# Optimization experiments

Hardware: AMD Instinct MI355X
Metric: run time of the kernel (lower is better)

Reference implementation:

```python
import jax, jax.numpy as jnp
import numpy as np

N = 50000      # nodes
E = 800000     # edges
IN = 128       # input features (arxiv)
HID = 128      # hidden per head
HEADS = 3      # arxiv_data=True -> 3 heads
OUT = 40       # classes
EPS = 1e-5     # BN eps
SLOPE = 0.2    # DGL GATConv leaky_relu negative slope


def setup_inputs() -> dict:
    key = jax.random.key(0)
    ks = jax.random.split(key, 20)
    x = jax.random.normal(ks[0], (N, IN), jnp.float32)
    src = jax.random.randint(ks[1], (E,), 0, N, dtype=jnp.int32)
    # guarantee every node has >=1 in-edge so edge_softmax is well-defined
    dst = jnp.concatenate([jnp.arange(N, dtype=jnp.int32),
                           jax.random.randint(ks[2], (E - N,), 0, N, dtype=jnp.int32)])

    def lin(k, fi, fo):
        return jax.random.normal(k, (fi, fo), jnp.float32) * (1.0 / np.sqrt(fi))

    def attn(k, h, d):
        return jax.random.normal(k, (h, d), jnp.float32) * 0.1

    return {
        "x": x, "src": src, "dst": dst,
        # layer 0: IN -> HEADS*HID
        "W0": lin(ks[3], IN, HEADS * HID),
        "al0": attn(ks[4], HEADS, HID), "ar0": attn(ks[5], HEADS, HID),
        "b0": jnp.zeros((HEADS * HID,), jnp.float32),
        # layer 1: HEADS*HID -> HEADS*HID
        "W1": lin(ks[6], HEADS * HID, HEADS * HID),
        "al1": attn(ks[7], HEADS, HID), "ar1": attn(ks[8], HEADS, HID),
        "b1": jnp.zeros((HEADS * HID,), jnp.float32),
        # layer 2: HEADS*HID -> OUT, 1 head
        "W2": lin(ks[9], HEADS * HID, OUT),
        "al2": attn(ks[10], 1, OUT), "ar2": attn(ks[11], 1, OUT),
        "b2": jnp.zeros((OUT,), jnp.float32),
        # batch norms over HEADS*HID channels
        "g0": jnp.ones((HEADS * HID,), jnp.float32), "be0": jnp.zeros((HEADS * HID,), jnp.float32),
        "g1": jnp.ones((HEADS * HID,), jnp.float32), "be1": jnp.zeros((HEADS * HID,), jnp.float32),
    }


def gat_layer(h, src, dst, W, al, ar, b, heads, d_out):
    # fc + per-head split: [N, heads, d_out]
    f = (h @ W).reshape(-1, heads, d_out)
    el = jnp.einsum('nhd,hd->nh', f, al)          # [N, H]
    er = jnp.einsum('nhd,hd->nh', f, ar)          # [N, H]
    e = jax.nn.leaky_relu(el[src] + er[dst], SLOPE)  # [E, H]
    # edge softmax over incoming edges of each dst node
    m = jax.ops.segment_max(e, dst, num_segments=N)
    ex = jnp.exp(e - m[dst])
    s = jax.ops.segment_sum(ex, dst, num_segments=N)
    a = ex / s[dst]                                # [E, H]
    # u_mul_e + sum aggregation
    out = jax.ops.segment_sum(f[src] * a[:, :, None], dst, num_segments=N)  # [N, H, D]
    out = out + b.reshape(1, heads, d_out)
    return out.reshape(-1, heads * d_out)


def batch_norm(h, g, b):
    mu = h.mean(axis=0)
    var = h.var(axis=0)
    return g * (h - mu) / jnp.sqrt(var + EPS) + b


def reference(x, src, dst, W0, al0, ar0, b0, W1, al1, ar1, b1,
              W2, al2, ar2, b2, g0, be0, g1, be1):
    h = gat_layer(x, src, dst, W0, al0, ar0, b0, HEADS, HID)
    h = jax.nn.relu(batch_norm(h, g0, be0))        # dropout: eval mode (identity)
    h = gat_layer(h, src, dst, W1, al1, ar1, b1, HEADS, HID)
    h = jax.nn.relu(batch_norm(h, g1, be1))
    out = gat_layer(h, src, dst, W2, al2, ar2, b2, 1, OUT)
    return out
```

## Files before the change

### kernel.cpp

```cpp
#include <hip/hip_runtime.h>
#include <hip/hip_bf16.h>

typedef __hip_bfloat16 bf16;
typedef __attribute__((ext_vector_type(8))) short short8;
typedef __attribute__((ext_vector_type(4))) float f32x4;

static constexpr int N_NODES  = 50000;
static constexpr int N_EDGES  = 800000;
static constexpr int F_IN     = 128;
static constexpr int D_HID    = 128;
static constexpr int H_HEADS  = 3;
static constexpr int F_OUT    = 40;
static constexpr int DEG_CAP  = 64;
static constexpr float BN_EPS = 1e-5f;
static constexpr float SLOPE  = 0.2f;

__device__ __forceinline__ float bfLo(unsigned int u) { return __uint_as_float(u << 16); }
__device__ __forceinline__ float bfHi(unsigned int u) { return __uint_as_float(u & 0xffff0000u); }
__device__ __forceinline__ float bfs(unsigned short s) { return __uint_as_float(((unsigned int)s) << 16); }
__device__ __forceinline__ unsigned int packbf(float a, float b) {
  union { bf16 h[2]; unsigned int u; } pk;
  pk.h[0] = __float2bfloat16(a);
  pk.h[1] = __float2bfloat16(b);
  return pk.u;
}
__device__ __forceinline__ short f2bf_s(float v) {
  bf16 h = __float2bfloat16(v);
  union { bf16 b; short s; } c; c.b = h; return c.s;
}
__device__ __forceinline__ void unpack_i8x4(unsigned int w, float* v) {
  v[0] = (float)(int)(char)(w & 0xff);
  v[1] = (float)(int)(char)((w >> 8) & 0xff);
  v[2] = (float)(int)(char)((w >> 16) & 0xff);
  v[3] = (float)(int)(char)((w >> 24) & 0xff);
}

__global__ __launch_bounds__(256) void gemm_mfma(const short* __restrict__ A,
                                                 const short* __restrict__ WT,
                                                 bf16* __restrict__ C,
                                                 const float* __restrict__ alp,
                                                 const float* __restrict__ arp,
                                                 float* __restrict__ el,
                                                 float* __restrict__ er,
                                                 const float* __restrict__ bnsrc,
                                                 const float* __restrict__ g,
                                                 const float* __restrict__ be,
                                                 float* __restrict__ bnstats,
                                                 int M, int K, int Nc, int els, int ers,
                                                 int lda, int ldc, int adiag) {
  constexpr int BM = 128, BN = 128, BK = 64, LDP = BK + 8;
  __shared__ short As[BM * LDP];
  __shared__ short Bs[BN * LDP];
  __shared__ float ecomb[128][4];
  __shared__ float sscale[384];
  __shared__ float sshift[384];
  int tid = threadIdx.x;
  int wave = tid >> 6, lane = tid & 63;
  int bm = blockIdx.y, bn = blockIdx.x;
  int m15 = lane & 15, quad = lane >> 4;
  int ksub = quad * 8;
  int wr = wave >> 1, wc = wave & 1;
  int srow = tid >> 3;
  int scol = (tid & 7) * 8;
  int acol0 = adiag ? bn * K : 0;

  if (bnsrc) {
    float inv_n = 1.f / (float)M;
    for (int c = tid; c < K; c += 256) {
      float mu = bnsrc[c] * inv_n;
      float var = bnsrc[K + c] * inv_n - mu * mu;
      float s = g[c] * rsqrtf(var + BN_EPS);
      sscale[c] = s;
      sshift[c] = be[c] - mu * s;
    }
    __syncthreads();
  }

  f32x4 acc[4][4];
#pragma unroll
  for (int i = 0; i < 4; ++i)
#pragma unroll
    for (int j = 0; j < 4; ++j) acc[i][j] = (f32x4){0.f, 0.f, 0.f, 0.f};

  for (int k0 = 0; k0 < K; k0 += BK) {
    int cb = k0 + scol;
    f32x4 sc0, sc1, sh0, sh1;
    if (bnsrc) {
      sc0 = *(const f32x4*)&sscale[cb]; sc1 = *(const f32x4*)&sscale[cb + 4];
      sh0 = *(const f32x4*)&sshift[cb]; sh1 = *(const f32x4*)&sshift[cb + 4];
    }
#pragma unroll
    for (int c = 0; c < 4; ++c) {
      int r = srow + c * 32;
      int gr = bm * BM + r; if (gr >= M) gr = M - 1;
      short8 av = *(const short8*)&A[(size_t)gr * lda + acol0 + k0 + scol];
      if (bnsrc) {
#pragma unroll
        for (int j = 0; j < 8; ++j) {
          float v = bfs((unsigned short)av[j]);
          float s = (j < 4) ? ((const float*)&sc0)[j] : ((const float*)&sc1)[j - 4];
          float t = (j < 4) ? ((const float*)&sh0)[j] : ((const float*)&sh1)[j - 4];
          float y = v * s + t;
          av[j] = f2bf_s(y > 0.f ? y : 0.f);
        }
      }
      *(short8*)&As[r * LDP + scol] = av;
      int gn = bn * BN + r;
      *(short8*)&Bs[r * LDP + scol] = *(const short8*)&WT[(size_t)gn * K + k0 + scol];
    }
    __syncthreads();
#pragma unroll
    for (int ks = 0; ks < BK; ks += 32) {
      short8 a[4], b[4];
#pragma unroll
      for (int i = 0; i < 4; ++i)
        a[i] = *(const short8*)&As[(wr * 64 + i * 16 + m15) * LDP + ks + ksub];
#pragma unroll
      for (int j = 0; j < 4; ++j)
        b[j] = *(const short8*)&Bs[(wc * 64 + j * 16 + m15) * LDP + ks + ksub];
#pragma unroll
      for (int i = 0; i < 4; ++i)
#pragma unroll
        for (int j = 0; j < 4; ++j)
          acc[i][j] = __builtin_amdgcn_mfma_f32_16x16x32_bf16(a[i], b[j], acc[i][j], 0, 0, 0);
    }
    __syncthreads();
  }

  int h = bn;
  float alv[4], arv[4];
#pragma unroll
  for (int j = 0; j < 4; ++j) {
    int col = bn * BN + wc * 64 + j * 16 + m15;
    alv[j] = alp[col];
    arv[j] = arp[col];
  }
  float csum[4] = {0.f, 0.f, 0.f, 0.f}, csq[4] = {0.f, 0.f, 0.f, 0.f};
#pragma unroll
  for (int i = 0; i < 4; ++i) {
#pragma unroll
    for (int r = 0; r < 4; ++r) {
      int rl = wr * 64 + i * 16 + quad * 4 + r;
      int row = bm * BM + rl;
      float pe = 0.f, pr = 0.f;
#pragma unroll
      for (int j = 0; j < 4; ++j) {
        float v = acc[i][j][r];
        pe += v * alv[j];
        pr += v * arv[j];
        if (bnstats && row < M) { csum[j] += v; csq[j] += v * v; }
        int col = bn * BN + wc * 64 + j * 16 + m15;
        if (row < M && col < Nc)
          C[(size_t)row * ldc + col] = __float2bfloat16(v);
      }
#pragma unroll
      for (int off = 1; off < 16; off <<= 1) {
        pe += __shfl_xor(pe, off);
        pr += __shfl_xor(pr, off);
      }
      if (m15 == 0) {
        ecomb[rl][wc] = pe;
        ecomb[rl][2 + wc] = pr;
      }
    }
  }
  if (bnstats) {
#pragma unroll
    for (int j = 0; j < 4; ++j) {
      csum[j] += __shfl_xor(csum[j], 16); csum[j] += __shfl_xor(csum[j], 32);
      csq[j]  += __shfl_xor(csq[j], 16);  csq[j]  += __shfl_xor(csq[j], 32);
    }
    if (quad == 0) {
#pragma unroll
      for (int j = 0; j < 4; ++j) {
        int col = bn * BN + wc * 64 + j * 16 + m15;
        atomicAdd(bnstats + col, csum[j]);
        atomicAdd(bnstats + Nc + col, csq[j]);
      }
    }
  }
  __syncthreads();
  if (tid < 128) {
    int row = bm * BM + tid;
    if (row < M) {
      el[(size_t)row * els + h] = ecomb[tid][0] + ecomb[tid][1];
      er[(size_t)row * ers + h] = ecomb[tid][2] + ecomb[tid][3];
    }
  }
}

__global__ void prep_kernel(const float* __restrict__ x, bf16* __restrict__ abuf,
                            const float* __restrict__ W0, const float* __restrict__ W1,
                            const float* __restrict__ W2, bf16* __restrict__ WT0,
                            bf16* __restrict__ WT1, bf16* __restrict__ WT2,
                            const float* __restrict__ al2, const float* __restrict__ ar2,
                            float* __restrict__ alp2, float* __restrict__ arp2,
                            int* __restrict__ fill, float* __restrict__ bnzero,
                            const float* __restrict__ al0, const float* __restrict__ ar0,
                            float* __restrict__ vl, float* __restrict__ vr) {
  const int NTOT = N_NODES * F_IN;
  for (int i = blockIdx.x * blockDim.x + threadIdx.x; i < NTOT;
       i += gridDim.x * blockDim.x) {
    abuf[i] = __float2bfloat16(x[i]);
    if (i < 384 * 384) { int n = i / 384, k = i - n * 384; WT1[i] = __float2bfloat16(W1[(size_t)k * 384 + n]); }
    if (i < 384 * 128) { int n = i / 128, k = i - n * 128; WT0[i] = __float2bfloat16(W0[(size_t)k * 384 + n]); }
    if (i < 128 * 384) { int n = i / 384, k = i - n * 384; WT2[i] = __float2bfloat16(n < F_OUT ? W2[(size_t)k * F_OUT + n] : 0.f); }
    if (i < N_NODES) fill[i] = 0;
    if (i < 4 * 384) bnzero[i] = 0.f;
    if (i < 128) { alp2[i] = i < F_OUT ? al2[i] : 0.f; arp2[i] = i < F_OUT ? ar2[i] : 0.f; }
  }
  if (blockIdx.x < 96) {
    int wid = blockIdx.x * 4 + (threadIdx.x >> 6);
    int lane = threadIdx.x & 63;
    int h = wid >> 7, k = wid & 127;
    const float2* wrow = (const float2*)(W0 + (size_t)k * 384 + h * 128);
    const float2* av = (const float2*)(al0 + h * 128);
    const float2* rv = (const float2*)(ar0 + h * 128);
    float2 wv = wrow[lane], a2 = av[lane], r2 = rv[lane];
    float sl = wv.x * a2.x + wv.y * a2.y;
    float sr = wv.x * r2.x + wv.y * r2.y;
#pragma unroll
    for (int off = 32; off > 0; off >>= 1) {
      sl += __shfl_xor(sl, off);
      sr += __shfl_xor(sr, off);
    }
    if (lane == 0) { vl[wid] = sl; vr[wid] = sr; }
  }
}

__global__ __launch_bounds__(256) void elr_kernel(const unsigned int* __restrict__ x2,
                                                  const float* __restrict__ vl,
                                                  const float* __restrict__ vr,
                                                  float* __restrict__ el,
                                                  float* __restrict__ er,
                                                  const int* __restrict__ src,
                                                  const int* __restrict__ dst,
                                                  int* __restrict__ fill,
                                                  int* __restrict__ bucket,
                                                  unsigned short* __restrict__ xq8,
                                                  float* __restrict__ xscale,
                                                  int N, int E) {
  int gid = blockIdx.x * 256 + threadIdx.x;
  if (gid < E) {
    int d = dst[gid];
    int pos = atomicAdd(fill + d, 1);
    if (pos < DEG_CAP) bucket[(size_t)d * DEG_CAP + pos] = src[gid];
  }
  int wv = threadIdx.x >> 6, lane = threadIdx.x & 63;
  int n = blockIdx.x * 4 + wv;
  if (n >= N) return;
  unsigned int u = x2[(size_t)n * 64 + lane];
  float v0 = bfLo(u), v1 = bfHi(u);
  float mx = fmaxf(fabsf(v0), fabsf(v1));
#pragma unroll
  for (int off = 32; off > 0; off >>= 1) mx = fmaxf(mx, __shfl_xor(mx, off));
  float qinv = mx > 0.f ? 127.f / mx : 0.f;
  int q0 = (int)rintf(v0 * qinv), q1 = (int)rintf(v1 * qinv);
  xq8[(size_t)n * 64 + lane] = (unsigned short)((q0 & 0xff) | ((q1 & 0xff) << 8));
  if (lane == 0) xscale[n] = mx * (1.f / 127.f);
  float pl[3], pr[3];
#pragma unroll
  for (int h = 0; h < 3; ++h) {
    float2 a2 = *(const float2*)&vl[h * 128 + 2 * lane];
    float2 r2 = *(const float2*)&vr[h * 128 + 2 * lane];
    pl[h] = v0 * a2.x + v1 * a2.y;
    pr[h] = v0 * r2.x + v1 * r2.y;
  }
#pragma unroll
  for (int h = 0; h < 3; ++h) {
#pragma unroll
    for (int off = 32; off > 0; off >>= 1) {
      pl[h] += __shfl_xor(pl[h], off);
      pr[h] += __shfl_xor(pr[h], off);
    }
  }
  if (lane == 0) {
    *(float4*)&el[(size_t)n * 4] = make_float4(pl[0], pl[1], pl[2], 0.f);
    er[(size_t)n * 3 + 0] = pr[0];
    er[(size_t)n * 3 + 1] = pr[1];
    er[(size_t)n * 3 + 2] = pr[2];
  }
}

__global__ __launch_bounds__(256) void quantf_kernel(const uint4* __restrict__ f4,
                                                     uint2* __restrict__ fq8,
                                                     float* __restrict__ fscale, int N) {
  int wv = threadIdx.x >> 6, lane = threadIdx.x & 63;
  int n = blockIdx.x * 4 + wv;
  if (n >= N) return;
  float v[8];
  float mx = 0.f;
  uint4 u;
  if (lane < 48) {
    u = f4[(size_t)n * 48 + lane];
    v[0] = bfLo(u.x); v[1] = bfHi(u.x);
    v[2] = bfLo(u.y); v[3] = bfHi(u.y);
    v[4] = bfLo(u.z); v[5] = bfHi(u.z);
    v[6] = bfLo(u.w); v[7] = bfHi(u.w);
#pragma unroll
    for (int j = 0; j < 8; ++j) mx = fmaxf(mx, fabsf(v[j]));
  }
#pragma unroll
  for (int off = 32; off > 0; off >>= 1) mx = fmaxf(mx, __shfl_xor(mx, off));
  float qinv = mx > 0.f ? 127.f / mx : 0.f;
  if (lane < 48) {
    int q[8];
#pragma unroll
    for (int j = 0; j < 8; ++j) q[j] = (int)rintf(v[j] * qinv);
    uint2 r;
    r.x = (q[0] & 0xff) | ((q[1] & 0xff) << 8) | ((q[2] & 0xff) << 16) | ((unsigned int)(q[3] & 0xff) << 24);
    r.y = (q[4] & 0xff) | ((q[5] & 0xff) << 8) | ((q[6] & 0xff) << 16) | ((unsigned int)(q[7] & 0xff) << 24);
    fq8[(size_t)n * 48 + lane] = r;
  }
  if (lane == 0) fscale[n] = mx * (1.f / 127.f);
}

__global__ __launch_bounds__(256) void aggr_x_kernel(
    const int* __restrict__ fill, const int* __restrict__ bucket,
    const float4* __restrict__ el4, const float* __restrict__ er,
    const uint2* __restrict__ xq, const float* __restrict__ xscale,
    uint4* __restrict__ outq, int N) {
  __shared__ float wls[4][64 * 3];
  __shared__ int   sls[4][64];
  int wv = threadIdx.x >> 6;
  int d = (blockIdx.x * 256 + threadIdx.x) >> 6;
  int lane = threadIdx.x & 63;
  if (d >= N) return;
  int deg = fill[d]; if (deg > DEG_CAP) deg = DEG_CAP;
  const int* myb = bucket + (size_t)d * DEG_CAP;
  float* mywls = wls[wv];
  int* mysls = sls[wv];
  int g = lane >> 4;
  int cch = lane & 15;

  float erd[3];
#pragma unroll
  for (int h = 0; h < 3; ++h) erd[h] = er[d * 3 + h];
  float acc[3][8];
#pragma unroll
  for (int h = 0; h < 3; ++h)
#pragma unroll
    for (int j = 0; j < 8; ++j) acc[h][j] = 0.f;
  float sp[3] = {0.f, 0.f, 0.f};

  if (lane < deg) {
    int s_l = myb[lane];
    mysls[lane] = s_l;
    float4 e4 = el4[s_l];
    float xs = xscale[s_l];
    float ev[3] = {e4.x, e4.y, e4.z};
#pragma unroll
    for (int h = 0; h < 3; ++h) {
      float sc = ev[h] + erd[h];
      sc = sc > 0.f ? sc : SLOPE * sc;
      float w = __expf(sc);
      mywls[lane * 3 + h] = w * xs;
      sp[h] += w;
    }
  }
  for (int e0 = 0; e0 < deg; e0 += 4) {
    int e = e0 + g;
    if (e < deg) {
      int se = mysls[e];
      float w0s = mywls[e * 3], w1s = mywls[e * 3 + 1], w2s = mywls[e * 3 + 2];
      uint2 u = xq[(size_t)se * 16 + cch];
      float ff[8];
      unpack_i8x4(u.x, ff);
      unpack_i8x4(u.y, ff + 4);
#pragma unroll
      for (int j = 0; j < 8; ++j) {
        acc[0][j] += w0s * ff[j];
        acc[1][j] += w1s * ff[j];
        acc[2][j] += w2s * ff[j];
      }
    }
  }
#pragma unroll
  for (int h = 0; h < 3; ++h) {
#pragma unroll
    for (int off = 32; off > 0; off >>= 1) sp[h] += __shfl_xor(sp[h], off);
  }
#pragma unroll
  for (int h = 0; h < 3; ++h)
#pragma unroll
    for (int j = 0; j < 8; ++j) {
      acc[h][j] += __shfl_xor(acc[h][j], 16);
      acc[h][j] += __shfl_xor(acc[h][j], 32);
    }
  if (g < 3) {
    float og[8];
#pragma unroll
    for (int j = 0; j < 8; ++j)
      og[j] = (g == 0) ? acc[0][j] : (g == 1) ? acc[1][j] : acc[2][j];
    float spg = (g == 0) ? sp[0] : (g == 1) ? sp[1] : sp[2];
    float inv = 1.f / spg;
    uint4 r;
    r.x = packbf(og[0] * inv, og[1] * inv);
    r.y = packbf(og[2] * inv, og[3] * inv);
    r.z = packbf(og[4] * inv, og[5] * inv);
    r.w = packbf(og[6] * inv, og[7] * inv);
    outq[(size_t)d * 48 + g * 16 + cch] = r;
  }
}

template <int H, int D>
__global__ __launch_bounds__(256) void aggr_fused_kernel(
    const int* __restrict__ fill, const int* __restrict__ bucket,
    const float4* __restrict__ el4, const float* __restrict__ er,
    const uint2* __restrict__ fq8, const float* __restrict__ fscale,
    uint4* __restrict__ outq, int N) {
  constexpr int WQ = H * D / 8;
  __shared__ float wls[4][64 * H];
  int wv = threadIdx.x >> 6;
  int d = (blockIdx.x * 256 + threadIdx.x) >> 6;
  int lane = threadIdx.x & 63;
  if (d >= N) return;
  int deg = fill[d]; if (deg > DEG_CAP) deg = DEG_CAP;
  const int* myb = bucket + (size_t)d * DEG_CAP;
  float* mywls = wls[wv];
  int hsel = lane >> 4;

  float erd[H];
#pragma unroll
  for (int h = 0; h < H; ++h) erd[h] = er[d * H + h];
  float acc[8];
#pragma unroll
  for (int j = 0; j < 8; ++j) acc[j] = 0.f;
  float sp[H];
#pragma unroll
  for (int h = 0; h < H; ++h) sp[h] = 0.f;

  int s_l = 0;
  if (lane < deg) {
    s_l = myb[lane];
    float4 e4 = el4[s_l];
    float fs = fscale[s_l];
    float ev[3] = {e4.x, e4.y, e4.z};
#pragma unroll
    for (int h = 0; h < H; ++h) {
      float sc = ev[h] + erd[h];
      sc = sc > 0.f ? sc : SLOPE * sc;
      float w = __expf(sc);
      mywls[lane * H + h] = w * fs;
      sp[h] += w;
    }
  }
  for (int e = 0; e < deg; ++e) {
    int se = __shfl(s_l, e);
    if (lane < WQ) {
      float w = mywls[e * H + hsel];
      uint2 u = fq8[(size_t)se * WQ + lane];
      float ff[8];
      unpack_i8x4(u.x, ff);
      unpack_i8x4(u.y, ff + 4);
      acc[0] += w * ff[0]; acc[1] += w * ff[1];
      acc[2] += w * ff[2]; acc[3] += w * ff[3];
      acc[4] += w * ff[4]; acc[5] += w * ff[5];
      acc[6] += w * ff[6]; acc[7] += w * ff[7];
    }
  }
#pragma unroll
  for (int h = 0; h < H; ++h) {
#pragma unroll
    for (int off = 32; off > 0; off >>= 1) sp[h] += __shfl_xor(sp[h], off);
  }
  if (lane < WQ) {
    float inv = 1.f / sp[hsel];
    uint4 r;
    r.x = packbf(acc[0] * inv, acc[1] * inv);
    r.y = packbf(acc[2] * inv, acc[3] * inv);
    r.z = packbf(acc[4] * inv, acc[5] * inv);
    r.w = packbf(acc[6] * inv, acc[7] * inv);
    outq[(size_t)d * WQ + lane] = r;
  }
}

__global__ __launch_bounds__(256) void aggr_out_kernel(
    const int* __restrict__ fill, const int* __restrict__ bucket,
    const float* __restrict__ el, const float* __restrict__ er,
    const bf16* __restrict__ f, const float* __restrict__ bias,
    float* __restrict__ out, int N) {
  constexpr int DW = F_OUT / 2;
  constexpr int LDW = 32;
  __shared__ float wls[4][64];
  __shared__ int   sls[4][64];
  int wv = threadIdx.x >> 6;
  int d = (blockIdx.x * 256 + threadIdx.x) >> 6;
  int lane = threadIdx.x & 63;
  if (d >= N) return;
  int deg = fill[d]; if (deg > DEG_CAP) deg = DEG_CAP;
  const int* myb = bucket + (size_t)d * DEG_CAP;
  const unsigned int* fu = (const unsigned int*)f;
  float* mywls = wls[wv];
  int* mysls = sls[wv];
  int g = lane / DW;
  int cch = lane - g * DW;
  float erd = er[d];
  float a0 = 0.f, a1 = 0.f, sp = 0.f;
  if (lane < deg) {
    int s_l = myb[lane];
    mysls[lane] = s_l;
    float sc = el[s_l] + erd;
    sc = sc > 0.f ? sc : SLOPE * sc;
    float w = __expf(sc);
    mywls[lane] = w;
    sp += w;
  }
  for (int e0 = 0; e0 < deg; e0 += 3) {
    int e = e0 + g;
    if (g < 3 && e < deg) {
      int se = mysls[e];
      float w = mywls[e];
      unsigned int u = fu[(size_t)se * LDW + cch];
      a0 += w * bfLo(u);
      a1 += w * bfHi(u);
    }
  }
#pragma unroll
  for (int off = 32; off > 0; off >>= 1) sp += __shfl_xor(sp, off);
  float b0 = __shfl(a0, (lane + DW) & 63), b1 = __shfl(a1, (lane + DW) & 63);
  float c0 = __shfl(a0, (lane + 2 * DW) & 63), c1 = __shfl(a1, (lane + 2 * DW) & 63);
  if (lane < DW) {
    float inv = 1.f / sp;
    float o0 = (a0 + b0 + c0) * inv + bias[2 * lane];
    float o1 = (a1 + b1 + c1) * inv + bias[2 * lane + 1];
    *(float2*)&out[(size_t)d * F_OUT + 2 * lane] = make_float2(o0, o1);
  }
}

__global__ void bn_stats_kernel(const unsigned int* __restrict__ h2, float* __restrict__ sum,
                                float* __restrict__ sumsq, int N, int C2) {
  int c = threadIdx.x;
  int step = gridDim.x;
  float s0 = 0.f, q0 = 0.f, s1 = 0.f, q1 = 0.f;
  int n = blockIdx.x;
  for (; n + 3 * step < N; n += 4 * step) {
    unsigned int ua = h2[(size_t)n * C2 + c];
    unsigned int ub = h2[(size_t)(n + step) * C2 + c];
    unsigned int uc = h2[(size_t)(n + 2 * step) * C2 + c];
    unsigned int ud = h2[(size_t)(n + 3 * step) * C2 + c];
    float va0 = bfLo(ua), va1 = bfHi(ua);
    float vb0 = bfLo(ub), vb1 = bfHi(ub);
    float vc0 = bfLo(uc), vc1 = bfHi(uc);
    float vd0 = bfLo(ud), vd1 = bfHi(ud);
    s0 += va0 + vb0 + vc0 + vd0;
    s1 += va1 + vb1 + vc1 + vd1;
    q0 += va0 * va0 + vb0 * vb0 + vc0 * vc0 + vd0 * vd0;
    q1 += va1 * va1 + vb1 * vb1 + vc1 * vc1 + vd1 * vd1;
  }
  for (; n < N; n += step) {
    unsigned int u = h2[(size_t)n * C2 + c];
    float v0 = bfLo(u), v1 = bfHi(u);
    s0 += v0; q0 += v0 * v0;
    s1 += v1; q1 += v1 * v1;
  }
  atomicAdd(sum + 2 * c, s0);
  atomicAdd(sum + 2 * c + 1, s1);
  atomicAdd(sumsq + 2 * c, q0);
  atomicAdd(sumsq + 2 * c + 1, q1);
}

static inline int cdiv(int a, int b) { return (a + b - 1) / b; }

extern "C" void kernel_launch(void* const* d_in, const int* in_sizes, int n_in,
                              void* d_out, int out_size, void* d_ws, size_t ws_size,
                              hipStream_t stream) {
  const float* x   = (const float*)d_in[0];
  const int* src   = (const int*)d_in[1];
  const int* dst   = (const int*)d_in[2];
  const float* W0  = (const float*)d_in[3];
  const float* al0 = (const float*)d_in[4];
  const float* ar0 = (const float*)d_in[5];
  const float* W1  = (const float*)d_in[7];
  const float* al1 = (const float*)d_in[8];
  const float* ar1 = (const float*)d_in[9];
  const float* W2  = (const float*)d_in[11];
  const float* al2 = (const float*)d_in[12];
  const float* ar2 = (const float*)d_in[13];
  const float* b2  = (const float*)d_in[14];
  const float* g0  = (const float*)d_in[15];
  const float* be0 = (const float*)d_in[16];
  const float* g1  = (const float*)d_in[17];
  const float* be1 = (const float*)d_in[18];
  float* out = (float*)d_out;

  const int N = N_NODES, E = N_EDGES, H = H_HEADS;
  const int C = H * D_HID;

  char* p = (char*)d_ws;
  auto take = [&](size_t bytes) {
    char* r = p;
    p += (bytes + 255) & ~(size_t)255;
    return r;
  };
  bf16*   f_buf   = (bf16*) take((size_t)N * C * sizeof(bf16));
  bf16*   hbuf    = (bf16*) take((size_t)N * C * sizeof(bf16));
  bf16*   abuf    = (bf16*) take((size_t)N * C * sizeof(bf16));
  float*  elbuf   = (float*)take((size_t)N * 4 * sizeof(float));
  float*  er      = (float*)take((size_t)N * H * sizeof(float));
  float*  bnbuf   = (float*)take((size_t)4 * C * sizeof(float));
  bf16*   WT0     = (bf16*) take((size_t)C * F_IN * sizeof(bf16));
  bf16*   WT1     = (bf16*) take((size_t)C * C * sizeof(bf16));
  bf16*   WT2     = (bf16*) take((size_t)128 * C * sizeof(bf16));
  float*  alp2    = (float*)take(128 * sizeof(float));
  float*  arp2    = (float*)take(128 * sizeof(float));
  float*  vlbuf   = (float*)take(384 * sizeof(float));
  float*  vrbuf   = (float*)take(384 * sizeof(float));
  int*    fill    = (int*)take((size_t)N * sizeof(int));
  int*    bucket  = (int*)take((size_t)N * DEG_CAP * sizeof(int));
  unsigned short* xq8 = (unsigned short*)take((size_t)N * 64 * sizeof(unsigned short));
  float*  xscale  = (float*)take((size_t)N * sizeof(float));
  uint2*  fq8     = (uint2*)take((size_t)N * 48 * sizeof(uint2));
  float*  fscale  = (float*)take((size_t)N * sizeof(float));
  float*  bnA = bnbuf;
  float*  bnB = bnbuf + 2 * C;

  prep_kernel<<<cdiv(N * F_IN, 256), 256, 0, stream>>>(x, abuf, W0, W1, W2, WT0, WT1, WT2,
                                                       al2, ar2, alp2, arp2, fill, bnbuf,
                                                       al0, ar0, vlbuf, vrbuf);
  elr_kernel<<<cdiv(N, 4), 256, 0, stream>>>((const unsigned int*)abuf, vlbuf, vrbuf,
                                             elbuf, er, src, dst, fill, bucket,
                                             xq8, xscale, N, E);

  aggr_x_kernel<<<cdiv(N * 64, 256), 256, 0, stream>>>(
      fill, bucket, (const float4*)elbuf, er, (const uint2*)xq8, xscale,
      (uint4*)f_buf, N);
  gemm_mfma<<<dim3(3, cdiv(N, 128)), 256, 0, stream>>>(
      (const short*)f_buf, (const short*)WT0, hbuf, al0, ar0, elbuf, er,
      nullptr, nullptr, nullptr, bnA, N, F_IN, C, 4, 3, C, C, 1);

  gemm_mfma<<<dim3(C / 128, cdiv(N, 128)), 256, 0, stream>>>(
      (const short*)hbuf, (const short*)WT1, f_buf, al1, ar1, elbuf, er,
      bnA, g0, be0, nullptr, N, C, C, 4, 3, C, C, 0);
  quantf_kernel<<<cdiv(N, 4), 256, 0, stream>>>((const uint4*)f_buf, fq8, fscale, N);
  aggr_fused_kernel<H_HEADS, D_HID><<<cdiv(N * 64, 256), 256, 0, stream>>>(
      fill, bucket, (const float4*)elbuf, er, fq8, fscale, (uint4*)hbuf, N);
  bn_stats_kernel<<<1024, C / 2, 0, stream>>>((const unsigned int*)hbuf, bnB, bnB + C, N, C / 2);

  gemm_mfma<<<dim3(1, cdiv(N, 128)), 256, 0, stream>>>(
      (const short*)hbuf, (const short*)WT2, f_buf, alp2, arp2, elbuf, er,
      bnB, g1, be1, nullptr, N, C, F_OUT, 1, 1, C, 64, 0);
  aggr_out_kernel<<<cdiv(N * 64, 256), 256, 0, stream>>>(
      fill, bucket, elbuf, er, f_buf, b2, out, N);
}
```

Before: 498.6 us.

## Fuse int8 quantization of layer-1 features into the GEMM epilogue

The layer-1 GEMM now quantizes its output straight to int8 in the epilogue, using a per-row, per-head absmax scale computed from the accumulators. This removes the bf16 write of f_buf and the separate quantf kernel launch that re-read it. The scale changes from one per node to one per head (128 columns), which changes numerics slightly. The aggregation kernel now reads a float4 of per-head scales. The int8 stores are byte-granular and strided, so the epilogue writes may be poorly coalesced.

```diff
diff --git a/kernel.cpp b/kernel.cpp
--- a/kernel.cpp
+++ b/kernel.cpp
@@ -46,12 +46,15 @@
                                                  const float* __restrict__ g,
                                                  const float* __restrict__ be,
                                                  float* __restrict__ bnstats,
+                                                 unsigned char* __restrict__ q8out,
+                                                 float* __restrict__ q8s,
                                                  int M, int K, int Nc, int els, int ers,
                                                  int lda, int ldc, int adiag) {
   constexpr int BM = 128, BN = 128, BK = 64, LDP = BK + 8;
   __shared__ short As[BM * LDP];
   __shared__ short Bs[BN * LDP];
   __shared__ float ecomb[128][4];
+  __shared__ float rmx[128][2];
   __shared__ float sscale[384];
   __shared__ float sshift[384];
   int tid = threadIdx.x;
@@ -136,6 +139,11 @@
     arv[j] = arp[col];
   }
   float csum[4] = {0.f, 0.f, 0.f, 0.f}, csq[4] = {0.f, 0.f, 0.f, 0.f};
+  float pm[4][4];
+#pragma unroll
+  for (int i = 0; i < 4; ++i)
+#pragma unroll
+    for (int r = 0; r < 4; ++r) pm[i][r] = 0.f;
 #pragma unroll
   for (int i = 0; i < 4; ++i) {
 #pragma unroll
@@ -149,8 +157,9 @@
         pe += v * alv[j];
         pr += v * arv[j];
         if (bnstats && row < M) { csum[j] += v; csq[j] += v * v; }
+        if (q8out) pm[i][r] = fmaxf(pm[i][r], fabsf(v));
         int col = bn * BN + wc * 64 + j * 16 + m15;
-        if (row < M && col < Nc)
+        if (!q8out && row < M && col < Nc)
           C[(size_t)row * ldc + col] = __float2bfloat16(v);
       }
 #pragma unroll
@@ -163,6 +172,17 @@
         ecomb[rl][2 + wc] = pr;
       }
     }
+  }
+  if (q8out) {
+#pragma unroll
+    for (int i = 0; i < 4; ++i)
+#pragma unroll
+      for (int r = 0; r < 4; ++r) {
+#pragma unroll
+        for (int off = 1; off < 16; off <<= 1)
+          pm[i][r] = fmaxf(pm[i][r], __shfl_xor(pm[i][r], off));
+        if (m15 == 0) rmx[wr * 64 + i * 16 + quad * 4 + r][wc] = pm[i][r];
+      }
   }
   if (bnstats) {
 #pragma unroll
@@ -180,11 +200,34 @@
     }
   }
   __syncthreads();
+  if (q8out) {
+#pragma unroll
+    for (int i = 0; i < 4; ++i)
+#pragma unroll
+      for (int r = 0; r < 4; ++r) {
+        int rl = wr * 64 + i * 16 + quad * 4 + r;
+        int row = bm * BM + rl;
+        float cm = fmaxf(rmx[rl][0], rmx[rl][1]);
+        float qinv = cm > 0.f ? 127.f / cm : 0.f;
+        if (row < M) {
+#pragma unroll
+          for (int j = 0; j < 4; ++j) {
+            int col = bn * BN + wc * 64 + j * 16 + m15;
+            int q = (int)rintf(acc[i][j][r] * qinv);
+            q8out[(size_t)row * 384 + col] = (unsigned char)(q & 0xff);
+          }
+        }
+      }
+  }
   if (tid < 128) {
     int row = bm * BM + tid;
     if (row < M) {
       el[(size_t)row * els + h] = ecomb[tid][0] + ecomb[tid][1];
       er[(size_t)row * ers + h] = ecomb[tid][2] + ecomb[tid][3];
+      if (q8out) {
+        float cm = fmaxf(rmx[tid][0], rmx[tid][1]);
+        q8s[(size_t)row * 4 + h] = cm * (1.f / 127.f);
+      }
     }
   }
 }
@@ -282,39 +325,6 @@
   }
 }
 
-__global__ __launch_bounds__(256) void quantf_kernel(const uint4* __restrict__ f4,
-                                                     uint2* __restrict__ fq8,
-                                                     float* __restrict__ fscale, int N) {
-  int wv = threadIdx.x >> 6, lane = threadIdx.x & 63;
-  int n = blockIdx.x * 4 + wv;
-  if (n >= N) return;
-  float v[8];
-  float mx = 0.f;
-  uint4 u;
-  if (lane < 48) {
-    u = f4[(size_t)n * 48 + lane];
-    v[0] = bfLo(u.x); v[1] = bfHi(u.x);
-    v[2] = bfLo(u.y); v[3] = bfHi(u.y);
-    v[4] = bfLo(u.z); v[5] = bfHi(u.z);
-    v[6] = bfLo(u.w); v[7] = bfHi(u.w);
-#pragma unroll
-    for (int j = 0; j < 8; ++j) mx = fmaxf(mx, fabsf(v[j]));
-  }
-#pragma unroll
-  for (int off = 32; off > 0; off >>= 1) mx = fmaxf(mx, __shfl_xor(mx, off));
-  float qinv = mx > 0.f ? 127.f / mx : 0.f;
-  if (lane < 48) {
-    int q[8];
-#pragma unroll
-    for (int j = 0; j < 8; ++j) q[j] = (int)rintf(v[j] * qinv);
-    uint2 r;
-    r.x = (q[0] & 0xff) | ((q[1] & 0xff) << 8) | ((q[2] & 0xff) << 16) | ((unsigned int)(q[3] & 0xff) << 24);
-    r.y = (q[4] & 0xff) | ((q[5] & 0xff) << 8) | ((q[6] & 0xff) << 16) | ((unsigned int)(q[7] & 0xff) << 24);
-    fq8[(size_t)n * 48 + lane] = r;
-  }
-  if (lane == 0) fscale[n] = mx * (1.f / 127.f);
-}
-
 __global__ __launch_bounds__(256) void aggr_x_kernel(
     const int* __restrict__ fill, const int* __restrict__ bucket,
     const float4* __restrict__ el4, const float* __restrict__ er,
@@ -407,7 +417,7 @@
 __global__ __launch_bounds__(256) void aggr_fused_kernel(
     const int* __restrict__ fill, const int* __restrict__ bucket,
     const float4* __restrict__ el4, const float* __restrict__ er,
-    const uint2* __restrict__ fq8, const float* __restrict__ fscale,
+    const uint2* __restrict__ fq8, const float4* __restrict__ fsc4,
     uint4* __restrict__ outq, int N) {
   constexpr int WQ = H * D / 8;
   __shared__ float wls[4][64 * H];
@@ -434,14 +444,15 @@
   if (lane < deg) {
     s_l = myb[lane];
     float4 e4 = el4[s_l];
-    float fs = fscale[s_l];
+    float4 fs = fsc4[s_l];
+    float fsv[3] = {fs.x, fs.y, fs.z};
     float ev[3] = {e4.x, e4.y, e4.z};
 #pragma unroll
     for (int h = 0; h < H; ++h) {
       float sc = ev[h] + erd[h];
       sc = sc > 0.f ? sc : SLOPE * sc;
       float w = __expf(sc);
-      mywls[lane * H + h] = w * fs;
+      mywls[lane * H + h] = w * fsv[h];
       sp[h] += w;
     }
   }
@@ -611,7 +622,7 @@
   unsigned short* xq8 = (unsigned short*)take((size_t)N * 64 * sizeof(unsigned short));
   float*  xscale  = (float*)take((size_t)N * sizeof(float));
   uint2*  fq8     = (uint2*)take((size_t)N * 48 * sizeof(uint2));
-  float*  fscale  = (float*)take((size_t)N * sizeof(float));
+  float*  fscale4 = (float*)take((size_t)N * 4 * sizeof(float));
   float*  bnA = bnbuf;
   float*  bnB = bnbuf + 2 * C;
 
@@ -627,19 +638,19 @@
       (uint4*)f_buf, N);
   gemm_mfma<<<dim3(3, cdiv(N, 128)), 256, 0, stream>>>(
       (const short*)f_buf, (const short*)WT0, hbuf, al0, ar0, elbuf, er,
-      nullptr, nullptr, nullptr, bnA, N, F_IN, C, 4, 3, C, C, 1);
+      nullptr, nullptr, nullptr, bnA, nullptr, nullptr, N, F_IN, C, 4, 3, C, C, 1);
 
   gemm_mfma<<<dim3(C / 128, cdiv(N, 128)), 256, 0, stream>>>(
-      (const short*)hbuf, (const short*)WT1, f_buf, al1, ar1, elbuf, er,
-      bnA, g0, be0, nullptr, N, C, C, 4, 3, C, C, 0);
-  quantf_kernel<<<cdiv(N, 4), 256, 0, stream>>>((const uint4*)f_buf, fq8, fscale, N);
+      (const short*)hbuf, (const short*)WT1, nullptr, al1, ar1, elbuf, er,
+      bnA, g0, be0, nullptr, (unsigned char*)fq8, fscale4, N, C, C, 4, 3, C, C, 0);
   aggr_fused_kernel<H_HEADS, D_HID><<<cdiv(N * 64, 256), 256, 0, stream>>>(
-      fill, bucket, (const float4*)elbuf, er, fq8, fscale, (uint4*)hbuf, N);
+      fill, bucket, (const float4*)elbuf, er, fq8, (const float4*)fscale4,
+      (uint4*)hbuf, N);
   bn_stats_kernel<<<1024, C / 2, 0, stream>>>((const unsigned int*)hbuf, bnB, bnB + C, N, C / 2);
 
   gemm_mfma<<<dim3(1, cdiv(N, 128)), 256, 0, stream>>>(
       (const short*)hbuf, (const short*)WT2, f_buf, alp2, arp2, elbuf, er,
-      bnB, g1, be1, nullptr, N, C, F_OUT, 1, 1, C, 64, 0);
+      bnB, g1, be1, nullptr, nullptr, nullptr, N, C, F_OUT, 1, 1, C, 64, 0);
   aggr_out_kernel<<<cdiv(N * 64, 256), 256, 0, stream>>>(
       fill, bucket, elbuf, er, f_buf, b2, out, N);
 }
```

Result: slower. 526.4 us (+5.6%).
